# Kernel optimization log

Hardware: AMD Instinct MI355X
Metric: run time of the kernel (lower is better)

## Reference

```python
import jax, jax.numpy as jnp
import numpy as np

NEG_INF = -1e6  # d2l masked_softmax mask value

def setup_inputs() -> dict:
    key = jax.random.key(0)
    ks = jax.random.split(key, 6)
    B, Lq, Lk, dq, dv, H = 8, 256, 512, 256, 256, 64
    return {
        "queries": jax.random.normal(ks[0], (B, Lq, dq), jnp.float32),
        "keys": jax.random.normal(ks[1], (B, Lk, dq), jnp.float32),
        "values": jax.random.normal(ks[2], (B, Lk, dv), jnp.float32),
        "valid_lens": jax.random.randint(ks[3], (B,), 0, Lk),
        "W_q": jax.random.normal(ks[4], (H, dq), jnp.float32) * (dq ** -0.5),
        "W_k": jax.random.normal(ks[5], (H, dq), jnp.float32) * (dq ** -0.5),
        "w_v": jax.random.normal(jax.random.fold_in(key, 7), (H,), jnp.float32) * (H ** -0.5),
    }

def reference(queries, keys, values, valid_lens, W_q, W_k, w_v):
    # Project: [B,Lq,H], [B,Lk,H]
    q = jnp.einsum('bqd,hd->bqh', queries, W_q)
    k = jnp.einsum('bkd,hd->bkh', keys, W_k)
    # Broadcast-add + tanh: [B,Lq,Lk,H]
    features = jnp.tanh(q[:, :, None, :] + k[:, None, :, :])
    # Scalar projection -> scores [B,Lq,Lk]
    scores = jnp.einsum('bqkh,h->bqk', features, w_v)
    # masked_softmax over last axis with per-batch valid_lens
    Lk = keys.shape[1]
    mask = jnp.arange(Lk)[None, None, :] < valid_lens[:, None, None]
    scores = jnp.where(mask, scores, NEG_INF)
    attn = jax.nn.softmax(scores, axis=-1)
    # dropout p=0 (inference) -> identity; bmm with values
    return jnp.einsum('bqk,bkv->bqv', attn, values)
```

## Files before the change

kernel.cpp:

```cpp
#include <hip/hip_runtime.h>
#include <hip/hip_bf16.h>
#include <hip/hip_fp16.h>
#include <stdint.h>

#define NB 8
#define LQ 256
#define LK 512
#define NH 64
#define SCALE 2.8853900817779268f
#define L2E 1.4426950408889634f

#define QP_OFF   0
#define KP_OFF   131072
#define VBF_OFF  393216
#define PML_OFF  917504

extern "C" __device__ float __ocml_exp2_f32(float);
static __device__ __forceinline__ float fexp2(float x) {
#if __has_builtin(__builtin_amdgcn_exp2f)
  return __builtin_amdgcn_exp2f(x);
#else
  return __ocml_exp2_f32(x);
#endif
}
static __device__ __forceinline__ float frcp(float x) {
  return __builtin_amdgcn_rcpf(x);
}
static __device__ __forceinline__ uint16_t f2bf(float f) {
  uint32_t u = __float_as_uint(f);
  uint32_t r = (u + 0x7FFFu + ((u >> 16) & 1u)) >> 16;
  return (uint16_t)r;
}

typedef const __attribute__((address_space(1))) void* gas_ptr;
typedef __attribute__((address_space(3))) void* las_ptr;
static __device__ __forceinline__ void gload16(const void* g, void* l) {
  __builtin_amdgcn_global_load_lds((gas_ptr)g, (las_ptr)l, 16, 0, 0);
}

__global__ __launch_bounds__(256) void proj_kernel(
    const float* __restrict__ queries, const float* __restrict__ keys,
    const float* __restrict__ values,
    const float* __restrict__ Wq, const float* __restrict__ Wk,
    float* __restrict__ qp, float* __restrict__ kp, uint16_t* __restrict__ vbf)
{
  __shared__ float Wt[256][36];
  const int blk = blockIdx.x;
  const int t = threadIdx.x;

  if (blk >= 384) {
    int base = (blk - 384) * 16384 + t * 4;
#pragma unroll
    for (int it = 0; it < 16; ++it) {
      int idx = base + it * 1024;
      float4 v = *(const float4*)(values + idx);
      uint32_t lo = (uint32_t)f2bf(v.x) | ((uint32_t)f2bf(v.y) << 16);
      uint32_t hi = (uint32_t)f2bf(v.z) | ((uint32_t)f2bf(v.w) << 16);
      uint2 pk = {lo, hi};
      *(uint2*)(vbf + idx) = pk;
    }
    return;
  }

  const bool isQ = (blk < 128);
  const int sub = isQ ? blk : (blk - 128);
  const int tile = sub >> 1;
  const int hh = (sub & 1) * 32;
  const int rowbase = tile * 32;
  const float* __restrict__ X = isQ ? queries : keys;
  const float* __restrict__ W = isQ ? Wq : Wk;
  float* __restrict__ P = isQ ? qp : kp;

#pragma unroll 4
  for (int it = 0; it < 32; ++it) {
    Wt[t][it] = W[(hh + it) * 256 + t];
  }
  __syncthreads();

  const int ty = t >> 4;
  const int tx = t & 15;
  float acc[2][2];
  acc[0][0] = acc[0][1] = acc[1][0] = acc[1][1] = 0.f;

  const float* xr0 = X + (rowbase + ty * 2 + 0) * 256;
  const float* xr1 = X + (rowbase + ty * 2 + 1) * 256;

#pragma unroll 4
  for (int d4 = 0; d4 < 64; ++d4) {
    int d = d4 * 4;
    float4 x0 = *(const float4*)(xr0 + d);
    float4 x1 = *(const float4*)(xr1 + d);
    float2 w0 = *(float2*)&Wt[d + 0][tx * 2];
    float2 w1 = *(float2*)&Wt[d + 1][tx * 2];
    float2 w2 = *(float2*)&Wt[d + 2][tx * 2];
    float2 w3 = *(float2*)&Wt[d + 3][tx * 2];
#define STEP(XC, WD) \
    acc[0][0] = fmaf(x0.XC, WD.x, acc[0][0]); acc[0][1] = fmaf(x0.XC, WD.y, acc[0][1]); \
    acc[1][0] = fmaf(x1.XC, WD.x, acc[1][0]); acc[1][1] = fmaf(x1.XC, WD.y, acc[1][1]);
    STEP(x, w0) STEP(y, w1) STEP(z, w2) STEP(w, w3)
#undef STEP
  }

#pragma unroll
  for (int i = 0; i < 2; ++i) {
    int row = rowbase + ty * 2 + i;
#pragma unroll
    for (int j = 0; j < 2; ++j) {
      int h = hh + tx * 2 + j;
      P[row * 64 + h] = acc[i][j] * SCALE;
    }
  }
}

__global__ __launch_bounds__(256) void attn_kernel(
    const float* __restrict__ qp, const float* __restrict__ kp,
    const uint16_t* __restrict__ vbf, const float* __restrict__ w_v,
    const int* __restrict__ valid_lens, float* __restrict__ out,
    float* __restrict__ pml, __half* __restrict__ pacc, int nsplit)
{
  __shared__ float kTs[2][32][64];
  __shared__ uint16_t Vs[2][32][256];
  __shared__ float q_s[4][2][64];
  __shared__ float w_s[64];
  __shared__ float p_s[4][2][32];

  const int t = threadIdx.x;
  const int lane = t & 63;
  const int w = t >> 6;
  const int r2 = lane >> 5;
  const int kj = lane & 31;
  const int wg = blockIdx.x;
  const int b = wg & 7;
  const int qg = (wg >> 3) & 31;
  const int kh = wg >> 8;
  const int row = b * LQ + qg * 8 + w * 2 + r2;

  const int vl = valid_lens[b];
  const int n = (vl > 0) ? vl : LK;
  const int span = LK / nsplit;
  const int kstart = kh * span;
  int cnt = n - kstart;
  if (cnt > span) cnt = span;
  const int ntiles = (cnt > 0) ? ((cnt + 31) >> 5) : 0;

  if (ntiles == 0) {
    if (kj == 0) {
      pml[(row * nsplit + kh) * 2 + 0] = -1e30f;
      pml[(row * nsplit + kh) * 2 + 1] = 0.f;
    }
    return;
  }

  {
    const float2* qsrc = (const float2*)(qp + (size_t)(b * LQ + qg * 8) * 64);
    ((float2*)q_s)[t] = qsrc[t];
    if (t < 64) w_s[t] = w_v[t];
  }

  float W1 = 0.f;
#pragma unroll
  for (int g = 0; g < 16; ++g) {
    float4 wf = *(const float4*)(w_v + g * 4);
    W1 += (wf.x + wf.y) + (wf.z + wf.w);
  }

  const float* kpb = kp + (size_t)(b * LK) * 64;
  const char* vbc = (const char*)(vbf + (size_t)b * LK * 256);

#define STAGE(BUF, K0) do { \
    int i0 = w * 2; \
    int kjr0 = i0 * 4 + (lane >> 4); \
    int cph = lane & 15; \
    gload16(kpb + (size_t)((K0) + kjr0) * 64 + (cph ^ (kjr0 & 7)) * 4, \
            &kTs[BUF][i0 * 4][0]); \
    int kjr1 = kjr0 + 4; \
    gload16(kpb + (size_t)((K0) + kjr1) * 64 + (cph ^ (kjr1 & 7)) * 4, \
            &kTs[BUF][i0 * 4 + 4][0]); \
    const char* vsrc = vbc + (size_t)(K0) * 512 + (size_t)w * 4096 + lane * 16; \
    gload16(vsrc + 0 * 1024, &Vs[BUF][w * 8 + 0][0]); \
    gload16(vsrc + 1 * 1024, &Vs[BUF][w * 8 + 2][0]); \
    gload16(vsrc + 2 * 1024, &Vs[BUF][w * 8 + 4][0]); \
    gload16(vsrc + 3 * 1024, &Vs[BUF][w * 8 + 6][0]); \
  } while (0)

  float m = -1e30f, l = 0.f;
  float acc[8];
#pragma unroll
  for (int i = 0; i < 8; ++i) acc[i] = 0.f;

  STAGE(0, kstart);
  __syncthreads();

  for (int tt = 0; tt < ntiles; ++tt) {
    const int cur = tt & 1;
    const int k0 = kstart + tt * 32;
    if (tt + 1 < ntiles) STAGE(cur ^ 1, k0 + 32);

    float r0 = 0.f, r1 = 0.f, r2a = 0.f, r3 = 0.f;
#pragma unroll
    for (int g = 0; g < 16; ++g) {
      float4 kf = *(const float4*)&kTs[cur][kj][((g ^ (kj & 7)) << 2)];
      float4 qf = *(const float4*)&q_s[w][r2][g * 4];
      float4 wf = *(const float4*)&w_s[g * 4];
      r0  = fmaf(wf.x, frcp(1.f + fexp2(qf.x + kf.x)), r0);
      r1  = fmaf(wf.y, frcp(1.f + fexp2(qf.y + kf.y)), r1);
      r2a = fmaf(wf.z, frcp(1.f + fexp2(qf.z + kf.z)), r2a);
      r3  = fmaf(wf.w, frcp(1.f + fexp2(qf.w + kf.w)), r3);
    }
    float racc = (r0 + r1) + (r2a + r3);

    float score;
    int kg = k0 + kj;
    if (vl == 0)      score = 0.f;
    else if (kg < n)  score = fmaf(-2.f, racc, W1);
    else              score = -1e30f;

    float mt = score;
#pragma unroll
    for (int s = 16; s; s >>= 1) mt = fmaxf(mt, __shfl_xor(mt, s, 64));
    float mnew = fmaxf(m, mt);
    float alpha = fexp2((m - mnew) * L2E);
    float p = fexp2((score - mnew) * L2E);
    m = mnew;
    float S = p;
#pragma unroll
    for (int s = 16; s; s >>= 1) S += __shfl_xor(S, s, 64);
    l = l * alpha + S;
    p_s[w][r2][kj] = p;

#pragma unroll
    for (int i = 0; i < 8; ++i) acc[i] *= alpha;
#pragma unroll
    for (int kj4 = 0; kj4 < 8; ++kj4) {
      float4 pf = *(const float4*)&p_s[w][r2][kj4 * 4];
#pragma unroll
      for (int jj = 0; jj < 4; ++jj) {
        int kk = kj4 * 4 + jj;
        uint4 vv = *(const uint4*)&Vs[cur][kk][kj * 8];
        float pj = (jj == 0) ? pf.x : (jj == 1) ? pf.y : (jj == 2) ? pf.z : pf.w;
        float f0 = __uint_as_float(vv.x << 16);
        float f1 = __uint_as_float(vv.x & 0xFFFF0000u);
        float f2 = __uint_as_float(vv.y << 16);
        float f3 = __uint_as_float(vv.y & 0xFFFF0000u);
        float f4 = __uint_as_float(vv.z << 16);
        float f5 = __uint_as_float(vv.z & 0xFFFF0000u);
        float f6 = __uint_as_float(vv.w << 16);
        float f7 = __uint_as_float(vv.w & 0xFFFF0000u);
        acc[0] = fmaf(pj, f0, acc[0]);
        acc[1] = fmaf(pj, f1, acc[1]);
        acc[2] = fmaf(pj, f2, acc[2]);
        acc[3] = fmaf(pj, f3, acc[3]);
        acc[4] = fmaf(pj, f4, acc[4]);
        acc[5] = fmaf(pj, f5, acc[5]);
        acc[6] = fmaf(pj, f6, acc[6]);
        acc[7] = fmaf(pj, f7, acc[7]);
      }
    }
    __syncthreads();
  }
#undef STAGE

  if (nsplit == 1) {
    float inv = 1.f / l;
    float4 o0 = {acc[0] * inv, acc[1] * inv, acc[2] * inv, acc[3] * inv};
    float4 o1 = {acc[4] * inv, acc[5] * inv, acc[6] * inv, acc[7] * inv};
    float* op = out + (size_t)row * 256 + kj * 8;
    *(float4*)(op + 0) = o0;
    *(float4*)(op + 4) = o1;
  } else {
    if (kj == 0) {
      pml[(row * nsplit + kh) * 2 + 0] = m;
      pml[(row * nsplit + kh) * 2 + 1] = l;
    }
    __half2 h0 = __floats2half2_rn(acc[0], acc[1]);
    __half2 h1 = __floats2half2_rn(acc[2], acc[3]);
    __half2 h2 = __floats2half2_rn(acc[4], acc[5]);
    __half2 h3 = __floats2half2_rn(acc[6], acc[7]);
    uint4 pk = {*(uint32_t*)&h0, *(uint32_t*)&h1, *(uint32_t*)&h2, *(uint32_t*)&h3};
    *(uint4*)(pacc + ((size_t)(row * nsplit + kh)) * 256 + kj * 8) = pk;
  }
}

__global__ __launch_bounds__(256) void merge_kernel(
    const float* __restrict__ pml, const __half* __restrict__ pacc,
    float* __restrict__ out, int nsplit)
{
  const int t = threadIdx.x;
  const int row = blockIdx.x * 8 + (t >> 5);
  const int d8 = t & 31;

  float ms = -1e30f;
  for (int kh = 0; kh < nsplit; ++kh)
    ms = fmaxf(ms, pml[(row * nsplit + kh) * 2]);

  float L = 0.f;
  float o[8];
#pragma unroll
  for (int i = 0; i < 8; ++i) o[i] = 0.f;

  for (int kh = 0; kh < nsplit; ++kh) {
    float mk = pml[(row * nsplit + kh) * 2 + 0];
    float lk = pml[(row * nsplit + kh) * 2 + 1];
    if (lk > 0.f) {
      float e = fexp2((mk - ms) * L2E);
      L += e * lk;
      uint4 pk = *(const uint4*)(pacc + ((size_t)(row * nsplit + kh)) * 256 + d8 * 8);
      __half2 h0 = *(__half2*)&pk.x, h1 = *(__half2*)&pk.y;
      __half2 h2 = *(__half2*)&pk.z, h3 = *(__half2*)&pk.w;
      float2 f0 = __half22float2(h0), f1 = __half22float2(h1);
      float2 f2 = __half22float2(h2), f3 = __half22float2(h3);
      o[0] = fmaf(e, f0.x, o[0]); o[1] = fmaf(e, f0.y, o[1]);
      o[2] = fmaf(e, f1.x, o[2]); o[3] = fmaf(e, f1.y, o[3]);
      o[4] = fmaf(e, f2.x, o[4]); o[5] = fmaf(e, f2.y, o[5]);
      o[6] = fmaf(e, f3.x, o[6]); o[7] = fmaf(e, f3.y, o[7]);
    }
  }
  float inv = 1.f / L;
  float4 o0 = {o[0] * inv, o[1] * inv, o[2] * inv, o[3] * inv};
  float4 o1 = {o[4] * inv, o[5] * inv, o[6] * inv, o[7] * inv};
  float* op = out + (size_t)row * 256 + d8 * 8;
  *(float4*)(op + 0) = o0;
  *(float4*)(op + 4) = o1;
}

extern "C" void kernel_launch(void* const* d_in, const int* in_sizes, int n_in,
                              void* d_out, int out_size, void* d_ws, size_t ws_size,
                              hipStream_t stream) {
  const float* queries    = (const float*)d_in[0];
  const float* keys       = (const float*)d_in[1];
  const float* values     = (const float*)d_in[2];
  const int*   valid_lens = (const int*)d_in[3];
  const float* Wq         = (const float*)d_in[4];
  const float* Wk         = (const float*)d_in[5];
  const float* w_v        = (const float*)d_in[6];
  float* out = (float*)d_out;

  float* ws = (float*)d_ws;
  float* qp  = ws + QP_OFF;
  float* kp  = ws + KP_OFF;
  uint16_t* vbf = (uint16_t*)(ws + VBF_OFF);
  float* pml = ws + PML_OFF;

  int nsplit;
  if      (ws_size >= (size_t)PML_OFF * 4 + 2048u * 4 * 8 + 2048u * 4 * 512) nsplit = 4;
  else if (ws_size >= (size_t)PML_OFF * 4 + 2048u * 2 * 8 + 2048u * 2 * 512) nsplit = 2;
  else nsplit = 1;
  __half* pacc = (__half*)(pml + (size_t)2048 * nsplit * 2);

  hipLaunchKernelGGL(proj_kernel, dim3(448), dim3(256), 0, stream,
                     queries, keys, values, Wq, Wk, qp, kp, vbf);
  hipLaunchKernelGGL(attn_kernel, dim3(nsplit * 256), dim3(256), 0, stream,
                     qp, kp, vbf, w_v, valid_lens, out, pml, pacc, nsplit);
  if (nsplit > 1) {
    hipLaunchKernelGGL(merge_kernel, dim3(256), dim3(256), 0, stream,
                       pml, pacc, out, nsplit);
  }
}
```

Before: 45.70 us.

## Stage X in LDS, read V directly from global, add split-8, manual barriers

The projection kernel now stages 16-row X tiles in shared memory and uses twice as many blocks, each computing one row per thread. The attention kernel stops staging V and w_v in LDS and reads them straight from global/L2. It replaces __syncthreads with explicit vmcnt waits, s_barrier and setprio for finer pipelining. An 8-way key split is enabled when workspace allows. This trades LDS traffic and occupancy limits for more global loads in the inner P·V loop, and adds more partial results for the merge kernel to combine.

```diff
diff --git a/kernel.cpp b/kernel.cpp
--- a/kernel.cpp
+++ b/kernel.cpp
@@ -44,12 +44,13 @@
     const float* __restrict__ Wq, const float* __restrict__ Wk,
     float* __restrict__ qp, float* __restrict__ kp, uint16_t* __restrict__ vbf)
 {
-  __shared__ float Wt[256][36];
+  __shared__ float Wt[256][34];
+  __shared__ float Xs[16][260];
   const int blk = blockIdx.x;
   const int t = threadIdx.x;
 
-  if (blk >= 384) {
-    int base = (blk - 384) * 16384 + t * 4;
+  if (blk >= 768) {
+    int base = (blk - 768) * 16384 + t * 4;
 #pragma unroll
     for (int it = 0; it < 16; ++it) {
       int idx = base + it * 1024;
@@ -62,11 +63,11 @@
     return;
   }
 
-  const bool isQ = (blk < 128);
-  const int sub = isQ ? blk : (blk - 128);
+  const bool isQ = (blk < 256);
+  const int sub = isQ ? blk : (blk - 256);
   const int tile = sub >> 1;
   const int hh = (sub & 1) * 32;
-  const int rowbase = tile * 32;
+  const int rowbase = tile * 16;
   const float* __restrict__ X = isQ ? queries : keys;
   const float* __restrict__ W = isQ ? Wq : Wk;
   float* __restrict__ P = isQ ? qp : kp;
@@ -75,40 +76,38 @@
   for (int it = 0; it < 32; ++it) {
     Wt[t][it] = W[(hh + it) * 256 + t];
   }
+#pragma unroll
+  for (int i = 0; i < 4; ++i) {
+    int flat4 = t + i * 256;
+    int r = flat4 >> 6, d4 = flat4 & 63;
+    float4 v = *(const float4*)(X + (size_t)(rowbase + r) * 256 + d4 * 4);
+    *(float4*)&Xs[r][d4 * 4] = v;
+  }
   __syncthreads();
 
   const int ty = t >> 4;
   const int tx = t & 15;
-  float acc[2][2];
-  acc[0][0] = acc[0][1] = acc[1][0] = acc[1][1] = 0.f;
-
-  const float* xr0 = X + (rowbase + ty * 2 + 0) * 256;
-  const float* xr1 = X + (rowbase + ty * 2 + 1) * 256;
+  float a0 = 0.f, a1 = 0.f;
 
 #pragma unroll 4
   for (int d4 = 0; d4 < 64; ++d4) {
     int d = d4 * 4;
-    float4 x0 = *(const float4*)(xr0 + d);
-    float4 x1 = *(const float4*)(xr1 + d);
+    float4 x0 = *(const float4*)&Xs[ty][d];
     float2 w0 = *(float2*)&Wt[d + 0][tx * 2];
     float2 w1 = *(float2*)&Wt[d + 1][tx * 2];
     float2 w2 = *(float2*)&Wt[d + 2][tx * 2];
     float2 w3 = *(float2*)&Wt[d + 3][tx * 2];
-#define STEP(XC, WD) \
-    acc[0][0] = fmaf(x0.XC, WD.x, acc[0][0]); acc[0][1] = fmaf(x0.XC, WD.y, acc[0][1]); \
-    acc[1][0] = fmaf(x1.XC, WD.x, acc[1][0]); acc[1][1] = fmaf(x1.XC, WD.y, acc[1][1]);
-    STEP(x, w0) STEP(y, w1) STEP(z, w2) STEP(w, w3)
-#undef STEP
-  }
-
-#pragma unroll
-  for (int i = 0; i < 2; ++i) {
-    int row = rowbase + ty * 2 + i;
-#pragma unroll
-    for (int j = 0; j < 2; ++j) {
-      int h = hh + tx * 2 + j;
-      P[row * 64 + h] = acc[i][j] * SCALE;
-    }
+    a0 = fmaf(x0.x, w0.x, a0); a1 = fmaf(x0.x, w0.y, a1);
+    a0 = fmaf(x0.y, w1.x, a0); a1 = fmaf(x0.y, w1.y, a1);
+    a0 = fmaf(x0.z, w2.x, a0); a1 = fmaf(x0.z, w2.y, a1);
+    a0 = fmaf(x0.w, w3.x, a0); a1 = fmaf(x0.w, w3.y, a1);
+  }
+
+  {
+    int row = rowbase + ty;
+    int h = hh + tx * 2;
+    P[row * 64 + h + 0] = a0 * SCALE;
+    P[row * 64 + h + 1] = a1 * SCALE;
   }
 }
 
@@ -119,16 +118,14 @@
     float* __restrict__ pml, __half* __restrict__ pacc, int nsplit)
 {
   __shared__ float kTs[2][32][64];
-  __shared__ uint16_t Vs[2][32][256];
   __shared__ float q_s[4][2][64];
-  __shared__ float w_s[64];
   __shared__ float p_s[4][2][32];
 
   const int t = threadIdx.x;
   const int lane = t & 63;
   const int w = t >> 6;
   const int r2 = lane >> 5;
-  const int kj = lane & 31;
+  const int kx = lane & 31;
   const int wg = blockIdx.x;
   const int b = wg & 7;
   const int qg = (wg >> 3) & 31;
@@ -144,7 +141,7 @@
   const int ntiles = (cnt > 0) ? ((cnt + 31) >> 5) : 0;
 
   if (ntiles == 0) {
-    if (kj == 0) {
+    if (kx == 0) {
       pml[(row * nsplit + kh) * 2 + 0] = -1e30f;
       pml[(row * nsplit + kh) * 2 + 1] = 0.f;
     }
@@ -154,7 +151,7 @@
   {
     const float2* qsrc = (const float2*)(qp + (size_t)(b * LQ + qg * 8) * 64);
     ((float2*)q_s)[t] = qsrc[t];
-    if (t < 64) w_s[t] = w_v[t];
+    asm volatile("s_waitcnt lgkmcnt(0)" ::: "memory");
   }
 
   float W1 = 0.f;
@@ -168,19 +165,13 @@
   const char* vbc = (const char*)(vbf + (size_t)b * LK * 256);
 
 #define STAGE(BUF, K0) do { \
-    int i0 = w * 2; \
-    int kjr0 = i0 * 4 + (lane >> 4); \
+    int r0_ = w * 4 + (lane >> 4); \
     int cph = lane & 15; \
-    gload16(kpb + (size_t)((K0) + kjr0) * 64 + (cph ^ (kjr0 & 7)) * 4, \
-            &kTs[BUF][i0 * 4][0]); \
-    int kjr1 = kjr0 + 4; \
-    gload16(kpb + (size_t)((K0) + kjr1) * 64 + (cph ^ (kjr1 & 7)) * 4, \
-            &kTs[BUF][i0 * 4 + 4][0]); \
-    const char* vsrc = vbc + (size_t)(K0) * 512 + (size_t)w * 4096 + lane * 16; \
-    gload16(vsrc + 0 * 1024, &Vs[BUF][w * 8 + 0][0]); \
-    gload16(vsrc + 1 * 1024, &Vs[BUF][w * 8 + 2][0]); \
-    gload16(vsrc + 2 * 1024, &Vs[BUF][w * 8 + 4][0]); \
-    gload16(vsrc + 3 * 1024, &Vs[BUF][w * 8 + 6][0]); \
+    gload16(kpb + (size_t)((K0) + r0_) * 64 + (cph ^ (r0_ & 7)) * 4, \
+            &kTs[BUF][w * 4][0]); \
+    int r1_ = r0_ + 16; \
+    gload16(kpb + (size_t)((K0) + r1_) * 64 + (cph ^ (r1_ & 7)) * 4, \
+            &kTs[BUF][w * 4 + 16][0]); \
   } while (0)
 
   float m = -1e30f, l = 0.f;
@@ -189,19 +180,27 @@
   for (int i = 0; i < 8; ++i) acc[i] = 0.f;
 
   STAGE(0, kstart);
-  __syncthreads();
 
   for (int tt = 0; tt < ntiles; ++tt) {
     const int cur = tt & 1;
     const int k0 = kstart + tt * 32;
-    if (tt + 1 < ntiles) STAGE(cur ^ 1, k0 + 32);
+    if (tt + 1 < ntiles) {
+      STAGE(cur ^ 1, k0 + 32);
+      asm volatile("s_waitcnt vmcnt(2)" ::: "memory");
+    } else {
+      asm volatile("s_waitcnt vmcnt(0)" ::: "memory");
+    }
+    __builtin_amdgcn_sched_barrier(0);
+    __builtin_amdgcn_s_barrier();
+    __builtin_amdgcn_sched_barrier(0);
+    __builtin_amdgcn_s_setprio(1);
 
     float r0 = 0.f, r1 = 0.f, r2a = 0.f, r3 = 0.f;
 #pragma unroll
     for (int g = 0; g < 16; ++g) {
-      float4 kf = *(const float4*)&kTs[cur][kj][((g ^ (kj & 7)) << 2)];
+      float4 kf = *(const float4*)&kTs[cur][kx][((g ^ (kx & 7)) << 2)];
       float4 qf = *(const float4*)&q_s[w][r2][g * 4];
-      float4 wf = *(const float4*)&w_s[g * 4];
+      float4 wf = *(const float4*)(w_v + g * 4);
       r0  = fmaf(wf.x, frcp(1.f + fexp2(qf.x + kf.x)), r0);
       r1  = fmaf(wf.y, frcp(1.f + fexp2(qf.y + kf.y)), r1);
       r2a = fmaf(wf.z, frcp(1.f + fexp2(qf.z + kf.z)), r2a);
@@ -210,7 +209,7 @@
     float racc = (r0 + r1) + (r2a + r3);
 
     float score;
-    int kg = k0 + kj;
+    int kg = k0 + kx;
     if (vl == 0)      score = 0.f;
     else if (kg < n)  score = fmaf(-2.f, racc, W1);
     else              score = -1e30f;
@@ -226,17 +225,18 @@
 #pragma unroll
     for (int s = 16; s; s >>= 1) S += __shfl_xor(S, s, 64);
     l = l * alpha + S;
-    p_s[w][r2][kj] = p;
+    p_s[w][r2][kx] = p;
 
 #pragma unroll
     for (int i = 0; i < 8; ++i) acc[i] *= alpha;
-#pragma unroll
-    for (int kj4 = 0; kj4 < 8; ++kj4) {
-      float4 pf = *(const float4*)&p_s[w][r2][kj4 * 4];
+    const int c = kx;
+#pragma unroll
+    for (int i4 = 0; i4 < 8; ++i4) {
+      float4 pf = *(const float4*)&p_s[w][r2][i4 * 4];
 #pragma unroll
       for (int jj = 0; jj < 4; ++jj) {
-        int kk = kj4 * 4 + jj;
-        uint4 vv = *(const uint4*)&Vs[cur][kk][kj * 8];
+        int kk = i4 * 4 + jj;
+        uint4 vv = *(const uint4*)(vbc + (size_t)(k0 + kk) * 512 + c * 16);
         float pj = (jj == 0) ? pf.x : (jj == 1) ? pf.y : (jj == 2) ? pf.z : pf.w;
         float f0 = __uint_as_float(vv.x << 16);
         float f1 = __uint_as_float(vv.x & 0xFFFF0000u);
@@ -256,7 +256,9 @@
         acc[7] = fmaf(pj, f7, acc[7]);
       }
     }
-    __syncthreads();
+    __builtin_amdgcn_s_setprio(0);
+    __builtin_amdgcn_sched_barrier(0);
+    __builtin_amdgcn_s_barrier();
   }
 #undef STAGE
 
@@ -264,11 +266,11 @@
     float inv = 1.f / l;
     float4 o0 = {acc[0] * inv, acc[1] * inv, acc[2] * inv, acc[3] * inv};
     float4 o1 = {acc[4] * inv, acc[5] * inv, acc[6] * inv, acc[7] * inv};
-    float* op = out + (size_t)row * 256 + kj * 8;
+    float* op = out + (size_t)row * 256 + kx * 8;
     *(float4*)(op + 0) = o0;
     *(float4*)(op + 4) = o1;
   } else {
-    if (kj == 0) {
+    if (kx == 0) {
       pml[(row * nsplit + kh) * 2 + 0] = m;
       pml[(row * nsplit + kh) * 2 + 1] = l;
     }
@@ -277,7 +279,7 @@
     __half2 h2 = __floats2half2_rn(acc[4], acc[5]);
     __half2 h3 = __floats2half2_rn(acc[6], acc[7]);
     uint4 pk = {*(uint32_t*)&h0, *(uint32_t*)&h1, *(uint32_t*)&h2, *(uint32_t*)&h3};
-    *(uint4*)(pacc + ((size_t)(row * nsplit + kh)) * 256 + kj * 8) = pk;
+    *(uint4*)(pacc + ((size_t)(row * nsplit + kh)) * 256 + kx * 8) = pk;
   }
 }
 
@@ -342,12 +344,13 @@
   float* pml = ws + PML_OFF;
 
   int nsplit;
-  if      (ws_size >= (size_t)PML_OFF * 4 + 2048u * 4 * 8 + 2048u * 4 * 512) nsplit = 4;
+  if      (ws_size >= (size_t)PML_OFF * 4 + 2048u * 8 * 8 + 2048u * 8 * 512) nsplit = 8;
+  else if (ws_size >= (size_t)PML_OFF * 4 + 2048u * 4 * 8 + 2048u * 4 * 512) nsplit = 4;
   else if (ws_size >= (size_t)PML_OFF * 4 + 2048u * 2 * 8 + 2048u * 2 * 512) nsplit = 2;
   else nsplit = 1;
   __half* pacc = (__half*)(pml + (size_t)2048 * nsplit * 2);
 
-  hipLaunchKernelGGL(proj_kernel, dim3(448), dim3(256), 0, stream,
+  hipLaunchKernelGGL(proj_kernel, dim3(832), dim3(256), 0, stream,
                      queries, keys, values, Wq, Wk, qp, kp, vbf);
   hipLaunchKernelGGL(attn_kernel, dim3(nsplit * 256), dim3(256), 0, stream,
                      qp, kp, vbf, w_v, valid_lens, out, pml, pacc, nsplit);
```

New measurement: 48.42 us. 5.9% more time.
